# Kernel optimization log

Hardware: AMD Instinct MI355X
Metric: run time of the kernel (lower is better)

Reference implementation:

```python
import jax, jax.numpy as jnp
import numpy as np

LN_EPS = 1e-5

def _ln(x, g, b):
    m = x.mean(-1, keepdims=True)
    v = x.var(-1, keepdims=True)
    return (x - m) * jax.lax.rsqrt(v + LN_EPS) * g + b

def _sru_layer(x, W, vc, bias, g, be):
    # x: (L, B, d); W: (d, k*h) with k=3 (d==h) or k=4 (d!=h)
    L, B, _ = x.shape
    h = vc.shape[0] // 2
    xn = _ln(x, g, be)
    k = W.shape[1] // h
    U = (xn @ W).reshape(L, B, k, h)
    u0, u1, u2 = U[:, :, 0], U[:, :, 1], U[:, :, 2]
    res = U[:, :, 3] if k == 4 else xn
    vf, vr = vc[:h], vc[h:]
    bf, br = bias[:h], bias[h:]
    def step(c, inp):
        a0, a1, a2, rt = inp
        f = jax.nn.sigmoid(a1 + vf * c + bf)
        r = jax.nn.sigmoid(a2 + vr * c + br)
        c2 = f * c + (1.0 - f) * a0
        return c2, r * c2 + (1.0 - r) * rt
    _, hs = jax.lax.scan(step, jnp.zeros((B, h), x.dtype), (u0, u1, u2, res))
    return hs  # (L, B, h)

def _lstm(x, Wih, Whh, bih, bhh):
    # x: (L, B, d); PyTorch gate order i, f, g, o
    L, B, _ = x.shape
    H = Whh.shape[1]
    pre = x @ Wih.T + (bih + bhh)  # (L, B, 4H)
    def step(carry, p):
        hp, cp = carry
        gates = p + hp @ Whh.T
        i, f, g, o = jnp.split(gates, 4, axis=-1)
        c = jax.nn.sigmoid(f) * cp + jax.nn.sigmoid(i) * jnp.tanh(g)
        hn = jax.nn.sigmoid(o) * jnp.tanh(c)
        return (hn, c), hn
    z = jnp.zeros((B, H), x.dtype)
    _, hs = jax.lax.scan(step, (z, z), pre)
    return hs

def setup_inputs() -> dict:
    key = jax.random.key(0)
    ks = jax.random.split(key, 12)
    B, T, F, H, LS, V = 16, 1024, 128, 1024, 1024, 1000
    s = 0.05
    inp = {}
    inp['x'] = jax.random.normal(ks[0], (B, T, F), dtype=jnp.float32)
    # first SRU layer (input F != H -> k=4)
    inp['w0'] = jax.random.normal(ks[1], (F, 4 * H), dtype=jnp.float32) * s
    inp['vc0'] = jax.random.normal(ks[2], (2 * H,), dtype=jnp.float32) * s
    inp['b0'] = jnp.zeros((2 * H,), jnp.float32)
    inp['g0'] = jnp.ones((F,), jnp.float32)
    inp['be0'] = jnp.zeros((F,), jnp.float32)
    # 6 stacked SRU layers with d==h (3 remaining first_layer + 3 sru_layers)
    inp['Ws'] = jax.random.normal(ks[3], (6, H, 3 * H), dtype=jnp.float32) * s
    inp['VCs'] = jax.random.normal(ks[4], (6, 2 * H), dtype=jnp.float32) * s
    inp['Bs'] = jnp.zeros((6, 2 * H), jnp.float32)
    inp['Gs'] = jnp.ones((6, H), jnp.float32)
    inp['Bes'] = jnp.zeros((6, H), jnp.float32)
    # LSTM
    inp['Wih'] = jax.random.normal(ks[5], (4 * LS, H), dtype=jnp.float32) * s
    inp['Whh'] = jax.random.normal(ks[6], (4 * LS, LS), dtype=jnp.float32) * s
    inp['bih'] = jnp.zeros((4 * LS,), jnp.float32)
    inp['bhh'] = jnp.zeros((4 * LS,), jnp.float32)
    # classifier: LayerNorm + Linear(no bias) to V+1
    inp['gh'] = jnp.ones((LS,), jnp.float32)
    inp['bh'] = jnp.zeros((LS,), jnp.float32)
    inp['Wout'] = jax.random.normal(ks[7], (LS, V + 1), dtype=jnp.float32) * s
    return inp

def reference(x, w0, vc0, b0, g0, be0, Ws, VCs, Bs, Gs, Bes,
              Wih, Whh, bih, bhh, gh, bh, Wout):
    t = jnp.transpose(x, (1, 0, 2))  # (T, B, F)
    t = _sru_layer(t, w0, vc0, b0, g0, be0)
    for i in range(3):
        t = _sru_layer(t, Ws[i], VCs[i], Bs[i], Gs[i], Bes[i])
    # AvgPool1d(kernel=2, stride=2) over time
    L = t.shape[0]
    t = t[: (L // 2) * 2].reshape(L // 2, 2, t.shape[1], t.shape[2]).mean(axis=1)
    for i in range(3, 6):
        t = _sru_layer(t, Ws[i], VCs[i], Bs[i], Gs[i], Bes[i])
    t = _lstm(t, Wih, Whh, bih, bhh)
    t = jnp.transpose(t, (1, 0, 2))  # (B, T/2, lstm_dim)
    return _ln(t, gh, bh) @ Wout  # (B, T/2, n_vocab+1)
```

## Files before the change

### kernel.cpp

```cpp
#include <hip/hip_runtime.h>

typedef __bf16 bf16x8 __attribute__((ext_vector_type(8)));
typedef float f32x4 __attribute__((ext_vector_type(4)));

__device__ __forceinline__ unsigned short f2bf(float f) {
  unsigned u = __builtin_bit_cast(unsigned, f);
  u += 0x7fffu + ((u >> 16) & 1u);
  return (unsigned short)(u >> 16);
}
__device__ __forceinline__ float bf2f(unsigned short h) {
  unsigned u = ((unsigned)h) << 16;
  return __builtin_bit_cast(float, u);
}
__device__ __forceinline__ float sigmoidf_(float x) {
  return 1.f / (1.f + __expf(-x));
}
__device__ __forceinline__ float tanhf_(float x) {
  return 1.f - 2.f / (__expf(2.f * x) + 1.f);
}
__device__ __forceinline__ void gload16(const unsigned short* g, unsigned short* l) {
  __builtin_amdgcn_global_load_lds((const __attribute__((address_space(1))) void*)g,
                                   (__attribute__((address_space(3))) void*)l, 16, 0, 0);
}


__global__ __launch_bounds__(256) void k_castf(const float* __restrict__ src,
                                               unsigned short* __restrict__ dst, int n4) {
  int i = blockIdx.x * 256 + threadIdx.x;
  if (i < n4) {
    float4 v = ((const float4*)src)[i];
    ushort4 o;
    o.x = f2bf(v.x); o.y = f2bf(v.y); o.z = f2bf(v.z); o.w = f2bf(v.w);
    ((ushort4*)dst)[i] = o;
  }
}

__global__ void k_cast_t(const float* __restrict__ src, unsigned short* __restrict__ dst,
                         int K, int N) {
  __shared__ float tile[32][33];
  int nx = blockIdx.x * 32, ky = blockIdx.y * 32;
  int tx = threadIdx.x, ty = threadIdx.y;
  #pragma unroll
  for (int j = 0; j < 32; j += 8) {
    int n = nx + tx, k = ky + ty + j;
    tile[ty + j][tx] = (n < N) ? src[(long)k * N + n] : 0.f;
  }
  __syncthreads();
  #pragma unroll
  for (int j = 0; j < 32; j += 8) {
    int n = nx + ty + j, k = ky + tx;
    dst[(long)n * K + k] = f2bf(tile[tx][ty + j]);
  }
}


__global__ __launch_bounds__(128) void k_ln0(const float* __restrict__ x,
                                             unsigned short* __restrict__ out,
                                             const float* __restrict__ g,
                                             const float* __restrict__ be) {
  int row = blockIdx.x;
  int t = row >> 4, b = row & 15;
  const float* src = x + ((long)b * 1024 + t) * 128;
  int i = threadIdx.x;
  float v = src[i];
  float s = v, q = v * v;
  #pragma unroll
  for (int off = 32; off > 0; off >>= 1) {
    s += __shfl_down(s, off);
    q += __shfl_down(q, off);
  }
  __shared__ float red[4];
  int wv = i >> 6;
  if ((i & 63) == 0) { red[wv] = s; red[2 + wv] = q; }
  __syncthreads();
  float S = red[0] + red[1], Q = red[2] + red[3];
  float mean = S * (1.f / 128.f);
  float var = Q * (1.f / 128.f) - mean * mean;
  float rs = rsqrtf(var + 1e-5f);
  out[(long)row * 128 + i] = f2bf((v - mean) * rs * g[i] + be[i]);
}

__global__ __launch_bounds__(256) void k_ln(const float* __restrict__ in,
                                            unsigned short* __restrict__ out16,
                                            const float* __restrict__ g,
                                            const float* __restrict__ be, int avg) {
  int row = blockIdx.x;
  int tid = threadIdx.x;
  int col = tid * 4;
  float xv[4];
  if (avg) {
    int l = row >> 4, b = row & 15;
    const float* r0 = in + ((long)(2 * l) * 16 + b) * 1024;
    const float* r1 = r0 + 16 * 1024;
    float4 a = *(const float4*)(r0 + col);
    float4 bb = *(const float4*)(r1 + col);
    xv[0] = 0.5f * (a.x + bb.x);
    xv[1] = 0.5f * (a.y + bb.y);
    xv[2] = 0.5f * (a.z + bb.z);
    xv[3] = 0.5f * (a.w + bb.w);
  } else {
    float4 a = *(const float4*)(in + (long)row * 1024 + col);
    xv[0] = a.x; xv[1] = a.y; xv[2] = a.z; xv[3] = a.w;
  }
  float s = xv[0] + xv[1] + xv[2] + xv[3];
  float q = xv[0]*xv[0] + xv[1]*xv[1] + xv[2]*xv[2] + xv[3]*xv[3];
  #pragma unroll
  for (int off = 32; off > 0; off >>= 1) {
    s += __shfl_down(s, off);
    q += __shfl_down(q, off);
  }
  __shared__ float red[8];
  int wv = tid >> 6;
  if ((tid & 63) == 0) { red[wv] = s; red[4 + wv] = q; }
  __syncthreads();
  float S = red[0] + red[1] + red[2] + red[3];
  float Q = red[4] + red[5] + red[6] + red[7];
  float mean = S * (1.f / 1024.f);
  float var = Q * (1.f / 1024.f) - mean * mean;
  float rs = rsqrtf(var + 1e-5f);
  ushort4 o;
  o.x = f2bf((xv[0] - mean) * rs * g[col + 0] + be[col + 0]);
  o.y = f2bf((xv[1] - mean) * rs * g[col + 1] + be[col + 1]);
  o.z = f2bf((xv[2] - mean) * rs * g[col + 2] + be[col + 2]);
  o.w = f2bf((xv[3] - mean) * rs * g[col + 3] + be[col + 3]);
  *(ushort4*)(out16 + (long)row * 1024 + col) = o;
}

template <int MODE>
__global__ __launch_bounds__(256) void k_gemm(const unsigned short* __restrict__ A,
                                              const unsigned short* __restrict__ Bt,
                                              void* __restrict__ Cout,
                                              const float* __restrict__ bias1,
                                              const float* __restrict__ bias2,
                                              int M, int N, int K) {
  __shared__ unsigned short As[128][64];
  __shared__ unsigned short Bs[128][64];
  const int nwg = gridDim.x * gridDim.y;
  const int bid = blockIdx.y * gridDim.x + blockIdx.x;
  const int swz = (bid & 7) * (nwg >> 3) + (bid >> 3);
  const int bn = (swz % gridDim.x) * 128, bm = (swz / gridDim.x) * 128;
  const int tid = threadIdx.x;
  const int wave = tid >> 6, lane = tid & 63;
  const int wm = (wave >> 1) * 64, wn = (wave & 1) * 64;
  const int l15 = lane & 15, kq = lane >> 4;
  f32x4 acc[4][4] = {};
  const int r0 = tid >> 3;
  const int c0 = (tid & 7) * 8;
  const unsigned short* Ap = A + (long)(bm + r0) * K + c0;
  const unsigned short* Bp = Bt + (long)(bn + r0) * K + c0;
  for (int kb = 0; kb < K; kb += 64) {
    #pragma unroll
    for (int i = 0; i < 4; i++) {
      gload16(Ap + (long)(i * 32) * K + kb, &As[i * 32 + r0][c0]);
      gload16(Bp + (long)(i * 32) * K + kb, &Bs[i * 32 + r0][c0]);
    }
    __syncthreads();
    #pragma unroll
    for (int kk = 0; kk < 2; kk++) {
      const int kcol = kk * 32 + kq * 8;
      bf16x8 a[4], b[4];
      #pragma unroll
      for (int m = 0; m < 4; m++) a[m] = *(const bf16x8*)&As[wm + m * 16 + l15][kcol];
      #pragma unroll
      for (int n = 0; n < 4; n++) b[n] = *(const bf16x8*)&Bs[wn + n * 16 + l15][kcol];
      #pragma unroll
      for (int m = 0; m < 4; m++)
        #pragma unroll
        for (int n = 0; n < 4; n++)
          acc[m][n] = __builtin_amdgcn_mfma_f32_16x16x32_bf16(a[m], b[n], acc[m][n], 0, 0, 0);
    }
    __syncthreads();
  }
  #pragma unroll
  for (int m = 0; m < 4; m++)
    #pragma unroll
    for (int n = 0; n < 4; n++) {
      #pragma unroll
      for (int r = 0; r < 4; r++) {
        int gm = bm + wm + m * 16 + kq * 4 + r;
        int gn = bn + wn + n * 16 + l15;
        float v = acc[m][n][r];
        if (MODE == 0) {
          ((float*)Cout)[(long)gm * N + gn] = v;
        } else if (MODE == 1) {
          v += bias1[gn] + bias2[gn];
          ((float*)Cout)[(long)gm * N + gn] = v;
        } else {
          if (gn < 1001) {
            long oi = ((long)(gm & 15) * 512 + (gm >> 4)) * 1001 + gn;
            ((float*)Cout)[oi] = v;
          }
        }
      }
    }
}

__global__ __launch_bounds__(64) void k_scan(const float* __restrict__ U,
                                             const unsigned short* __restrict__ Res16,
                                             const float* __restrict__ vc,
                                             const float* __restrict__ bias,
                                             float* __restrict__ Hout,
                                             unsigned short* __restrict__ H16,
                                             float* __restrict__ cbuf,
                                             int Lc, int k4, int first) {
  int tid = blockIdx.x * 64 + threadIdx.x;
  int b = tid >> 10, hc = tid & 1023;
  float vf = vc[hc], vr = vc[1024 + hc];
  float bfv = bias[hc], brv = bias[1024 + hc];
  const int k = k4 ? 4 : 3;
  const long strideT = 16L * k * 1024;
  const long base0 = (long)b * k * 1024 + hc;
  const long rbase = (long)b * 1024 + hc;
  const long rstride = 16 * 1024;
  float c = first ? 0.f : cbuf[tid];
  for (int t0 = 0; t0 < Lc; t0 += 16) {
    float u0[16], u1[16], u2[16], rr[16];
    #pragma unroll
    for (int j = 0; j < 16; j++) {
      long o = base0 + (long)(t0 + j) * strideT;
      u0[j] = U[o];
      u1[j] = U[o + 1024];
      u2[j] = U[o + 2048];
      rr[j] = k4 ? U[o + 3072] : bf2f(Res16[rbase + (long)(t0 + j) * rstride]);
    }
    #pragma unroll
    for (int j = 0; j < 16; j++) {
      float f = sigmoidf_(u1[j] + vf * c + bfv);
      float r = sigmoidf_(u2[j] + vr * c + brv);
      c = f * c + (1.f - f) * u0[j];
      float h = r * c + (1.f - r) * rr[j];
      long oo = rbase + (long)(t0 + j) * rstride;
      if (Hout) Hout[oo] = h;
      if (H16) H16[oo] = f2bf(h);
    }
  }
  cbuf[tid] = c;
}

__global__ __launch_bounds__(256) void k_lstm_step(
    const unsigned short* __restrict__ Whhb,
    const float* __restrict__ Prep,
    const unsigned short* __restrict__ hin,
    unsigned short* __restrict__ hout,
    float* __restrict__ cst,
    float* __restrict__ HsOutp) {
  const int tid = threadIdx.x;
  const int wave = tid >> 6, lane = tid & 63;
  const int j = blockIdx.x;
  const int c0 = j * 4;
  const int l15 = lane & 15, kq = lane >> 4;
  const int wrow = (l15 >> 2) * 1024 + c0 + (l15 & 3);
  const int pm = tid >> 4, pcol = tid & 15;
  float pre = Prep[(long)pm * 4096 + (pcol >> 2) * 1024 + c0 + (pcol & 3)];
  float cold = 0.f;
  long ci = 0;
  if (tid < 64) {
    int m = tid & 15, chl = tid >> 4;
    ci = (long)m * 1024 + c0 + chl;
    cold = cst[ci];
  }
  f32x4 acc = {0.f, 0.f, 0.f, 0.f};
  const unsigned short* hp = hin + l15 * 1024 + wave * 256 + kq * 8;
  const unsigned short* wp = Whhb + (long)wrow * 1024 + wave * 256 + kq * 8;
  #pragma unroll
  for (int kb = 0; kb < 256; kb += 32) {
    bf16x8 a = *(const bf16x8*)(hp + kb);
    bf16x8 w = *(const bf16x8*)(wp + kb);
    acc = __builtin_amdgcn_mfma_f32_16x16x32_bf16(a, w, acc, 0, 0, 0);
  }
  __shared__ float P[4][16][16];
  __shared__ float G[16][16];
  #pragma unroll
  for (int r = 0; r < 4; r++) {
    int m = kq * 4 + r;
    P[wave][m][l15] = acc[r];
  }
  __syncthreads();
  G[pm][pcol] = P[0][pm][pcol] + P[1][pm][pcol] + P[2][pm][pcol] + P[3][pm][pcol] + pre;
  __syncthreads();
  if (tid < 64) {
    int m = tid & 15, chl = tid >> 4;
    float ig = G[m][0 * 4 + chl];
    float fg = G[m][1 * 4 + chl];
    float gg = G[m][2 * 4 + chl];
    float og = G[m][3 * 4 + chl];
    float cn = sigmoidf_(fg) * cold + sigmoidf_(ig) * tanhf_(gg);
    float hn = sigmoidf_(og) * tanhf_(cn);
    cst[ci] = cn;
    hout[ci] = f2bf(hn);
    HsOutp[ci] = hn;
  }
}


extern "C" void kernel_launch(void* const* d_in, const int* in_sizes, int n_in,
                              void* d_out, int out_size, void* d_ws, size_t ws_size,
                              hipStream_t stream) {
  const float* x    = (const float*)d_in[0];
  const float* w0   = (const float*)d_in[1];
  const float* vc0  = (const float*)d_in[2];
  const float* b0   = (const float*)d_in[3];
  const float* g0   = (const float*)d_in[4];
  const float* be0  = (const float*)d_in[5];
  const float* Ws   = (const float*)d_in[6];
  const float* VCs  = (const float*)d_in[7];
  const float* Bsi  = (const float*)d_in[8];
  const float* Gs   = (const float*)d_in[9];
  const float* Bes  = (const float*)d_in[10];
  const float* Wih  = (const float*)d_in[11];
  const float* Whh  = (const float*)d_in[12];
  const float* bih  = (const float*)d_in[13];
  const float* bhh  = (const float*)d_in[14];
  const float* gh   = (const float*)d_in[15];
  const float* bh   = (const float*)d_in[16];
  const float* Wout = (const float*)d_in[17];

  char* ws = (char*)d_ws;
  size_t off = 0;
  auto alloc = [&](size_t bytes) {
    size_t r = off;
    off += (bytes + 255) & ~(size_t)255;
    return r;
  };
  unsigned short* W0t   = (unsigned short*)(ws + alloc(4096UL * 128 * 2));
  unsigned short* Wst   = (unsigned short*)(ws + alloc(6UL * 3072 * 1024 * 2));
  unsigned short* Wihb  = (unsigned short*)(ws + alloc(4096UL * 1024 * 2));
  unsigned short* Whhb  = (unsigned short*)(ws + alloc(4096UL * 1024 * 2));
  unsigned short* Woutt = (unsigned short*)(ws + alloc(1024UL * 1024 * 2));
  unsigned short* Xn    = (unsigned short*)(ws + alloc(16384UL * 1024 * 2));
  float*          Hbuf  = (float*)(ws + alloc(16384UL * 1024 * 4));
  float*          Ubuf  = (float*)(ws + alloc(4096UL * 4096 * 4));
  unsigned short* hb0   = (unsigned short*)(ws + alloc(16UL * 1024 * 2));
  unsigned short* hb1   = (unsigned short*)(ws + alloc(16UL * 1024 * 2));
  float*          cst   = (float*)(ws + alloc(16UL * 1024 * 4));
  float*          cscan = (float*)(ws + alloc(16UL * 1024 * 4));
  float*          HsOut = Hbuf;
  unsigned short* H16l6 = Xn + 8192L * 1024;
  unsigned short* LNout = Xn;

  k_cast_t<<<dim3(4096 / 32, 128 / 32), dim3(32, 8), 0, stream>>>(w0, W0t, 128, 4096);
  for (int i = 0; i < 6; i++)
    k_cast_t<<<dim3(3072 / 32, 1024 / 32), dim3(32, 8), 0, stream>>>(
        Ws + (long)i * 1024 * 3072, Wst + (long)i * 3072 * 1024, 1024, 3072);
  k_cast_t<<<dim3(1024 / 32, 1024 / 32), dim3(32, 8), 0, stream>>>(Wout, Woutt, 1024, 1001);
  k_castf<<<4096, 256, 0, stream>>>(Wih, Wihb, 4096 * 1024 / 4);
  k_castf<<<4096, 256, 0, stream>>>(Whh, Whhb, 4096 * 1024 / 4);
  hipMemsetAsync(hb0, 0, 32768 + 32768 + 65536, stream);

  const int CH_T = 256;
  const int CH_R = CH_T * 16;

  k_ln0<<<16384, 128, 0, stream>>>(x, Xn, g0, be0);
  for (int c = 0; c < 4; c++) {
    k_gemm<0><<<dim3(4096 / 128, CH_R / 128), 256, 0, stream>>>(
        Xn + (long)c * CH_R * 128, W0t, Ubuf, nullptr, nullptr, CH_R, 4096, 128);
    k_scan<<<256, 64, 0, stream>>>(Ubuf, nullptr, vc0, b0,
                                   Hbuf + (long)c * CH_R * 1024, nullptr, cscan,
                                   CH_T, 1, c == 0);
  }

  for (int i = 0; i < 6; i++) {
    int L = (i < 3) ? 1024 : 512;
    int rows = L * 16;
    int avg = (i == 3) ? 1 : 0;
    k_ln<<<rows, 256, 0, stream>>>(Hbuf, Xn, Gs + i * 1024, Bes + i * 1024, avg);
    int nch = rows / CH_R;
    for (int c = 0; c < nch; c++) {
      k_gemm<0><<<dim3(3072 / 128, CH_R / 128), 256, 0, stream>>>(
          Xn + (long)c * CH_R * 1024, Wst + (long)i * 3072 * 1024, Ubuf, nullptr, nullptr,
          CH_R, 3072, 1024);
      k_scan<<<256, 64, 0, stream>>>(Ubuf, Xn + (long)c * CH_R * 1024,
                                     VCs + i * 2048, Bsi + i * 2048,
                                     (i == 5) ? nullptr : (Hbuf + (long)c * CH_R * 1024),
                                     (i == 5) ? (H16l6 + (long)c * CH_R * 1024) : nullptr,
                                     cscan, CH_T, 0, c == 0);
    }
  }

  const int LCH_T = 256, LCH_R = LCH_T * 16;
  for (int c = 0; c < 2; c++) {
    k_gemm<1><<<dim3(4096 / 128, LCH_R / 128), 256, 0, stream>>>(
        H16l6 + (long)c * LCH_R * 1024, Wihb, Ubuf, bih, bhh, LCH_R, 4096, 1024);
    for (int tl = 0; tl < LCH_T; tl++) {
      int tg = c * LCH_T + tl;
      unsigned short* hin = (tg & 1) ? hb1 : hb0;
      unsigned short* hout = (tg & 1) ? hb0 : hb1;
      k_lstm_step<<<256, 256, 0, stream>>>(Whhb, Ubuf + (long)tl * 16 * 4096, hin, hout,
                                           cst, HsOut + (long)tg * 16 * 1024);
    }
  }

  k_ln<<<8192, 256, 0, stream>>>(HsOut, LNout, gh, bh, 0);
  k_gemm<2><<<dim3(1024 / 128, 8192 / 128), 256, 0, stream>>>(LNout, Woutt, d_out, nullptr,
                                                              nullptr, 8192, 1024, 1024);
}
```

Measured before the change: 6.158 ms.

## Overlap SRU scan of previous chunk with GEMM of next chunk in one kernel

Adds a combined kernel in which the first 64 blocks run the sequential SRU scan for chunk c-1 while the remaining blocks compute the projection GEMM for chunk c. The U buffer is double-buffered so the two stages can run concurrently. The aim is to hide the latency-bound, low-occupancy scan behind GEMM work instead of serialising them. The first layer now uses smaller time chunks to allow more overlap. The cost is a larger workspace, and the 256-thread scan blocks may be scheduled late relative to the GEMM blocks.

```diff
diff --git a/kernel.cpp b/kernel.cpp
--- a/kernel.cpp
+++ b/kernel.cpp
@@ -195,6 +195,100 @@
     }
 }
 
+__global__ __launch_bounds__(256) void k_gemm_scan(
+    const unsigned short* __restrict__ A, const unsigned short* __restrict__ Bt,
+    float* __restrict__ Cout, int M, int N, int K,
+    const float* __restrict__ sU, const unsigned short* __restrict__ sRes16,
+    const float* __restrict__ vc, const float* __restrict__ bias,
+    float* __restrict__ sHout, unsigned short* __restrict__ sH16,
+    float* __restrict__ cbuf, int Lc, int k4, int sfirst) {
+  __shared__ unsigned short As[128][64];
+  __shared__ unsigned short Bs[128][64];
+  const int bid = blockIdx.x;
+  const int tid = threadIdx.x;
+  if (bid < 64) {
+    int sid = bid * 256 + tid;
+    int b = sid >> 10, hc = sid & 1023;
+    float vf = vc[hc], vr = vc[1024 + hc];
+    float bfv = bias[hc], brv = bias[1024 + hc];
+    const int k = k4 ? 4 : 3;
+    const long strideT = 16L * k * 1024;
+    const long base0 = (long)b * k * 1024 + hc;
+    const long rbase = (long)b * 1024 + hc;
+    const long rstride = 16 * 1024;
+    float c = sfirst ? 0.f : cbuf[sid];
+    for (int t0 = 0; t0 < Lc; t0 += 16) {
+      float u0[16], u1[16], u2[16], rr[16];
+      #pragma unroll
+      for (int j = 0; j < 16; j++) {
+        long o = base0 + (long)(t0 + j) * strideT;
+        u0[j] = sU[o];
+        u1[j] = sU[o + 1024];
+        u2[j] = sU[o + 2048];
+        rr[j] = k4 ? sU[o + 3072] : bf2f(sRes16[rbase + (long)(t0 + j) * rstride]);
+      }
+      #pragma unroll
+      for (int j = 0; j < 16; j++) {
+        float f = sigmoidf_(u1[j] + vf * c + bfv);
+        float r = sigmoidf_(u2[j] + vr * c + brv);
+        c = f * c + (1.f - f) * u0[j];
+        float h = r * c + (1.f - r) * rr[j];
+        long oo = rbase + (long)(t0 + j) * rstride;
+        if (sHout) sHout[oo] = h;
+        if (sH16) sH16[oo] = f2bf(h);
+      }
+    }
+    cbuf[sid] = c;
+    return;
+  }
+  const int gb = bid - 64;
+  const int ntile = N >> 7;
+  const int nwg = (M >> 7) * ntile;
+  const int swz = (gb & 7) * (nwg >> 3) + (gb >> 3);
+  const int bn = (swz % ntile) * 128, bm = (swz / ntile) * 128;
+  const int wave = tid >> 6, lane = tid & 63;
+  const int wm = (wave >> 1) * 64, wn = (wave & 1) * 64;
+  const int l15 = lane & 15, kq = lane >> 4;
+  f32x4 acc[4][4] = {};
+  const int r0 = tid >> 3;
+  const int c0 = (tid & 7) * 8;
+  const unsigned short* Ap = A + (long)(bm + r0) * K + c0;
+  const unsigned short* Bp = Bt + (long)(bn + r0) * K + c0;
+  for (int kb = 0; kb < K; kb += 64) {
+    #pragma unroll
+    for (int i = 0; i < 4; i++) {
+      gload16(Ap + (long)(i * 32) * K + kb, &As[i * 32 + r0][c0]);
+      gload16(Bp + (long)(i * 32) * K + kb, &Bs[i * 32 + r0][c0]);
+    }
+    __syncthreads();
+    #pragma unroll
+    for (int kk = 0; kk < 2; kk++) {
+      const int kcol = kk * 32 + kq * 8;
+      bf16x8 a[4], b[4];
+      #pragma unroll
+      for (int m = 0; m < 4; m++) a[m] = *(const bf16x8*)&As[wm + m * 16 + l15][kcol];
+      #pragma unroll
+      for (int n = 0; n < 4; n++) b[n] = *(const bf16x8*)&Bs[wn + n * 16 + l15][kcol];
+      #pragma unroll
+      for (int m = 0; m < 4; m++)
+        #pragma unroll
+        for (int n = 0; n < 4; n++)
+          acc[m][n] = __builtin_amdgcn_mfma_f32_16x16x32_bf16(a[m], b[n], acc[m][n], 0, 0, 0);
+    }
+    __syncthreads();
+  }
+  #pragma unroll
+  for (int m = 0; m < 4; m++)
+    #pragma unroll
+    for (int n = 0; n < 4; n++)
+      #pragma unroll
+      for (int r = 0; r < 4; r++) {
+        int gm = bm + wm + m * 16 + kq * 4 + r;
+        int gn = bn + wn + n * 16 + l15;
+        Cout[(long)gm * N + gn] = acc[m][n][r];
+      }
+}
+
 __global__ __launch_bounds__(64) void k_scan(const float* __restrict__ U,
                                              const unsigned short* __restrict__ Res16,
                                              const float* __restrict__ vc,
@@ -329,11 +423,12 @@
   unsigned short* Woutt = (unsigned short*)(ws + alloc(1024UL * 1024 * 2));
   unsigned short* Xn    = (unsigned short*)(ws + alloc(16384UL * 1024 * 2));
   float*          Hbuf  = (float*)(ws + alloc(16384UL * 1024 * 4));
-  float*          Ubuf  = (float*)(ws + alloc(4096UL * 4096 * 4));
+  float*          Ubuf  = (float*)(ws + alloc(2UL * 4096 * 3072 * 4));
   unsigned short* hb0   = (unsigned short*)(ws + alloc(16UL * 1024 * 2));
   unsigned short* hb1   = (unsigned short*)(ws + alloc(16UL * 1024 * 2));
   float*          cst   = (float*)(ws + alloc(16UL * 1024 * 4));
   float*          cscan = (float*)(ws + alloc(16UL * 1024 * 4));
+  const long U_HALF = 4096L * 3072;
   float*          HsOut = Hbuf;
   unsigned short* H16l6 = Xn + 8192L * 1024;
   unsigned short* LNout = Xn;
@@ -347,34 +442,56 @@
   k_castf<<<4096, 256, 0, stream>>>(Whh, Whhb, 4096 * 1024 / 4);
   hipMemsetAsync(hb0, 0, 32768 + 32768 + 65536, stream);
 
-  const int CH_T = 256;
-  const int CH_R = CH_T * 16;
-
-  k_ln0<<<16384, 128, 0, stream>>>(x, Xn, g0, be0);
-  for (int c = 0; c < 4; c++) {
-    k_gemm<0><<<dim3(4096 / 128, CH_R / 128), 256, 0, stream>>>(
-        Xn + (long)c * CH_R * 128, W0t, Ubuf, nullptr, nullptr, CH_R, 4096, 128);
-    k_scan<<<256, 64, 0, stream>>>(Ubuf, nullptr, vc0, b0,
-                                   Hbuf + (long)c * CH_R * 1024, nullptr, cscan,
-                                   CH_T, 1, c == 0);
-  }
-
+  {
+    const int T0 = 128, R0 = T0 * 16;
+    k_ln0<<<16384, 128, 0, stream>>>(x, Xn, g0, be0);
+    for (int c = 0; c < 8; c++) {
+      float* Uc = Ubuf + (c & 1) * U_HALF;
+      if (c == 0) {
+        k_gemm<0><<<dim3(4096 / 128, R0 / 128), 256, 0, stream>>>(
+            Xn, W0t, Uc, nullptr, nullptr, R0, 4096, 128);
+      } else {
+        k_gemm_scan<<<64 + (4096 / 128) * (R0 / 128), 256, 0, stream>>>(
+            Xn + (long)c * R0 * 128, W0t, Uc, R0, 4096, 128,
+            Ubuf + ((c - 1) & 1) * U_HALF, nullptr, vc0, b0,
+            Hbuf + (long)(c - 1) * R0 * 1024, nullptr, cscan, T0, 1, c == 1);
+      }
+    }
+    k_scan<<<256, 64, 0, stream>>>(Ubuf + (7 & 1) * U_HALF, nullptr, vc0, b0,
+                                   Hbuf + 7L * R0 * 1024, nullptr, cscan, T0, 1, 0);
+  }
+
+  const int CH_T = 256, CH_R = CH_T * 16;
   for (int i = 0; i < 6; i++) {
     int L = (i < 3) ? 1024 : 512;
     int rows = L * 16;
     int avg = (i == 3) ? 1 : 0;
     k_ln<<<rows, 256, 0, stream>>>(Hbuf, Xn, Gs + i * 1024, Bes + i * 1024, avg);
     int nch = rows / CH_R;
+    const unsigned short* Wb = Wst + (long)i * 3072 * 1024;
     for (int c = 0; c < nch; c++) {
-      k_gemm<0><<<dim3(3072 / 128, CH_R / 128), 256, 0, stream>>>(
-          Xn + (long)c * CH_R * 1024, Wst + (long)i * 3072 * 1024, Ubuf, nullptr, nullptr,
-          CH_R, 3072, 1024);
-      k_scan<<<256, 64, 0, stream>>>(Ubuf, Xn + (long)c * CH_R * 1024,
-                                     VCs + i * 2048, Bsi + i * 2048,
-                                     (i == 5) ? nullptr : (Hbuf + (long)c * CH_R * 1024),
-                                     (i == 5) ? (H16l6 + (long)c * CH_R * 1024) : nullptr,
-                                     cscan, CH_T, 0, c == 0);
-    }
+      float* Uc = Ubuf + (c & 1) * U_HALF;
+      if (c == 0) {
+        k_gemm<0><<<dim3(3072 / 128, CH_R / 128), 256, 0, stream>>>(
+            Xn, Wb, Uc, nullptr, nullptr, CH_R, 3072, 1024);
+      } else {
+        int sc = c - 1;
+        k_gemm_scan<<<64 + (3072 / 128) * (CH_R / 128), 256, 0, stream>>>(
+            Xn + (long)c * CH_R * 1024, Wb, Uc, CH_R, 3072, 1024,
+            Ubuf + (sc & 1) * U_HALF, Xn + (long)sc * CH_R * 1024,
+            VCs + i * 2048, Bsi + i * 2048,
+            (i == 5) ? nullptr : (Hbuf + (long)sc * CH_R * 1024),
+            (i == 5) ? (H16l6 + (long)sc * CH_R * 1024) : nullptr,
+            cscan, CH_T, 0, sc == 0);
+      }
+    }
+    int sc = nch - 1;
+    k_scan<<<256, 64, 0, stream>>>(Ubuf + (sc & 1) * U_HALF,
+                                   Xn + (long)sc * CH_R * 1024,
+                                   VCs + i * 2048, Bsi + i * 2048,
+                                   (i == 5) ? nullptr : (Hbuf + (long)sc * CH_R * 1024),
+                                   (i == 5) ? (H16l6 + (long)sc * CH_R * 1024) : nullptr,
+                                   cscan, CH_T, 0, sc == 0);
   }
 
   const int LCH_T = 256, LCH_R = LCH_T * 16;
```

After: 5.676 ms. -7.8%, faster.
